# Kernel tuning notes

Hardware: AMD Instinct MI355X
Metric: run time of the kernel (lower is better)

The kernel has to match this reference:

```python
import jax, jax.numpy as jnp
import numpy as np


def setup_inputs() -> dict:
    key = jax.random.key(0)
    ks = jax.random.split(key, 5)
    t, b, s, d = 4, 4, 1024, 512
    x = jax.random.normal(ks[0], (t, b, s, d), dtype=jnp.float32)
    wq = jax.random.normal(ks[1], (d, d), dtype=jnp.float32) * 0.02
    wk = jax.random.normal(ks[2], (d, d), dtype=jnp.float32) * 0.02
    wv = jax.random.normal(ks[3], (d, d), dtype=jnp.float32) * 0.02
    wo = jax.random.normal(ks[4], (d, d), dtype=jnp.float32) * 0.02
    z = jnp.zeros((d,), dtype=jnp.float32)
    return {"x": x, "wq": wq, "bq": z, "wk": wk, "bk": z, "wv": wv,
            "bv": z, "wo": wo, "bo": z, "num_heads": 8}


def reference(x, wq, bq, wk, bk, wv, bv, wo, bo, num_heads):
    t, b, s, d = x.shape
    dh = d // num_heads
    # QKV projections (torch Linear stores weight as [out,in]; here weights are
    # random square matrices so x @ w + b is the same math)
    q = x @ wq + bq
    k = x @ wk + bk
    v = x @ wv + bv
    # Faithful to source: plain row-major view to (t*b*h, s, dh) WITHOUT
    # transposing a head axis (this mixes seq blocks into the batch-of-heads dim)
    q = q.reshape(t * b * num_heads, s, dh)
    k = k.reshape(t * b * num_heads, s, dh)
    v = v.reshape(t * b * num_heads, s, dh)
    scale = 1.0 / jnp.sqrt(jnp.float32(dh))
    scores = jnp.einsum('bqd,bkd->bqk', q, k) * scale  # [t*b*h, s, s]
    attn = jax.nn.softmax(scores, axis=-1)
    out = jnp.einsum('bqk,bkd->bqd', attn, v)  # [t*b*h, s, dh]
    out = out.reshape(t, b, s, d)
    return out @ wo + bo
```

## Files before the change

kernel.cpp:

```cpp
#include <hip/hip_runtime.h>

typedef __bf16 bf16;
typedef __bf16 bf16x4 __attribute__((ext_vector_type(4)));
typedef __bf16 bf16x8 __attribute__((ext_vector_type(8)));
typedef float  f32x4  __attribute__((ext_vector_type(4)));

#define MFMA16(a, b, c) __builtin_amdgcn_mfma_f32_16x16x32_bf16((a), (b), (c), 0, 0, 0)
#define SW(row, g) (((row) << 6) + ((((g) ^ ((row) & 7))) << 3))

#define QSCALE 0.1803368801111137f

typedef __attribute__((address_space(3))) uint32_t       lds_u32_t;
typedef const __attribute__((address_space(1))) uint32_t glob_u32_t;

__device__ __forceinline__ void ld_lds16(const bf16* g, bf16* l) {
    __builtin_amdgcn_global_load_lds((glob_u32_t*)g, (lds_u32_t*)l, 16, 0, 0);
}

__global__ __launch_bounds__(256) void prep(
    const float* __restrict__ X,
    const float* __restrict__ wq, const float* __restrict__ wk,
    const float* __restrict__ wv, const float* __restrict__ wo,
    bf16* __restrict__ Xb, bf16* __restrict__ wqkvT, bf16* __restrict__ woT)
{
    int bid = blockIdx.x;
    if (bid < 4096) {
        size_t i = ((size_t)bid * 256 + threadIdx.x) * 8;
        const f32x4* s = (const f32x4*)(X + i);
        f32x4 a = s[0], b = s[1];
        bf16x8 o;
        for (int e = 0; e < 4; e++) { o[e] = (bf16)a[e]; o[e + 4] = (bf16)b[e]; }
        *(bf16x8*)(Xb + i) = o;
    } else {
        int idx = (bid - 4096) * 256 + threadIdx.x;
        int which = idx >> 15;
        int r = idx & 32767;
        int kg = r >> 9, n = r & 511;
        const float* w = (which == 0) ? wq : (which == 1) ? wk : (which == 2) ? wv : wo;
        bf16x8 o;
        for (int e = 0; e < 8; e++) o[e] = (bf16)w[(size_t)(kg * 8 + e) * 512 + n];
        bf16* dst = ((which < 3) ? (wqkvT + (size_t)which * 262144) : woT) + (size_t)n * 512 + kg * 8;
        *(bf16x8*)dst = o;
    }
}

__global__ __launch_bounds__(256, 4) void gemm_qkv(
    const bf16* __restrict__ Xb, const bf16* __restrict__ WT,
    const float* __restrict__ bq, const float* __restrict__ bk,
    const float* __restrict__ bv,
    bf16* __restrict__ Q, bf16* __restrict__ K, bf16* __restrict__ V)
{
    __shared__ char smem[34816];
    bf16* As = (bf16*)smem;
    bf16* Bs = (bf16*)(smem + 16384);

    const int t = threadIdx.x;
    const int lane = t & 63, wid = t >> 6;
    const int wr = wid >> 1, wc = wid & 1;
    const int lr = lane & 15, quad = lane >> 4;
    const int bid = blockIdx.x;
    const int xcd = bid & 7, j0 = bid >> 3;
    const int m0 = (xcd * 16 + (j0 & 15)) * 128;
    const int x = j0 >> 4;
    const int which = x >> 2;
    const int n0 = (x & 3) * 128;
    const bf16* Wt = WT + (size_t)which * 262144;

    f32x4 zf = {0.f, 0.f, 0.f, 0.f};
    f32x4 acc[4][4];
    for (int i = 0; i < 4; i++)
        for (int jj = 0; jj < 4; jj++) acc[i][jj] = zf;

    const int srow = t >> 3;
    const int sg = (t & 7) ^ (srow & 7);
    const bf16* gA = Xb + (size_t)(m0 + srow) * 512 + sg * 8;
    const bf16* gB = Wt + (size_t)(n0 + srow) * 512 + sg * 8;
    bf16* lA = As + t * 8;
    bf16* lB = Bs + t * 8;

    for (int k0 = 0; k0 < 512; k0 += 64) {
        for (int p = 0; p < 4; p++) {
            ld_lds16(gA + k0 + p * 32 * 512, lA + p * 2048);
            ld_lds16(gB + k0 + p * 32 * 512, lB + p * 2048);
        }
        __syncthreads();
        for (int kk = 0; kk < 2; ++kk) {
            bf16x8 af[4], bf_[4];
            for (int i = 0; i < 4; i++)
                af[i] = *(const bf16x8*)&As[SW(wr * 64 + i * 16 + lr, kk * 4 + quad)];
            for (int jj = 0; jj < 4; jj++)
                bf_[jj] = *(const bf16x8*)&Bs[SW(wc * 64 + jj * 16 + lr, kk * 4 + quad)];
            for (int i = 0; i < 4; i++)
                for (int jj = 0; jj < 4; jj++)
                    acc[i][jj] = MFMA16(af[i], bf_[jj], acc[i][jj]);
        }
        __syncthreads();
    }

    bf16* OUT = (which == 0) ? Q : (which == 1) ? K : V;
    const float* bias = (which == 0) ? bq : (which == 1) ? bk : bv;
    const float qs = (which == 0) ? QSCALE : 1.0f;

    bf16* Ep = (bf16*)smem + wid * 4352;
    for (int jj = 0; jj < 4; jj++) {
        int n = n0 + wc * 64 + jj * 16 + lr;
        float bb = bias[n];
        for (int i = 0; i < 4; i++) {
            int row = i * 16 + quad * 4;
            for (int r = 0; r < 4; r++)
                Ep[(row + r) * 68 + jj * 16 + lr] = (bf16)((acc[i][jj][r] + bb) * qs);
        }
    }
    bf16* wO = OUT + (size_t)(m0 + wr * 64) * 512 + n0 + wc * 64;
    for (int s = 0; s < 8; s++) {
        int row = s * 8 + (lane >> 3), g = lane & 7;
        *(bf16x8*)(wO + (size_t)row * 512 + g * 8) = *(const bf16x8*)&Ep[row * 68 + g * 8];
    }
}

__global__ __launch_bounds__(256, 4) void gemm_out(
    const bf16* __restrict__ A, const bf16* __restrict__ WoT,
    const float* __restrict__ bo, float* __restrict__ OUT)
{
    __shared__ char smem[34816];
    bf16* As = (bf16*)smem;
    bf16* Bs = (bf16*)(smem + 16384);

    const int t = threadIdx.x;
    const int lane = t & 63, wid = t >> 6;
    const int wr = wid >> 1, wc = wid & 1;
    const int lr = lane & 15, quad = lane >> 4;
    const int bid = blockIdx.x;
    const int xcd = bid & 7, j0 = bid >> 3;
    const int m0 = (xcd * 16 + (j0 & 15)) * 128;
    const int n0 = (j0 >> 4) * 128;

    f32x4 zf = {0.f, 0.f, 0.f, 0.f};
    f32x4 acc[4][4];
    for (int i = 0; i < 4; i++)
        for (int jj = 0; jj < 4; jj++) acc[i][jj] = zf;

    const int srow = t >> 3;
    const int sg = (t & 7) ^ (srow & 7);
    const bf16* gA = A + (size_t)(m0 + srow) * 512 + sg * 8;
    const bf16* gB = WoT + (size_t)(n0 + srow) * 512 + sg * 8;
    bf16* lA = As + t * 8;
    bf16* lB = Bs + t * 8;

    for (int k0 = 0; k0 < 512; k0 += 64) {
        for (int p = 0; p < 4; p++) {
            ld_lds16(gA + k0 + p * 32 * 512, lA + p * 2048);
            ld_lds16(gB + k0 + p * 32 * 512, lB + p * 2048);
        }
        __syncthreads();
        for (int kk = 0; kk < 2; ++kk) {
            bf16x8 af[4], bf_[4];
            for (int i = 0; i < 4; i++)
                af[i] = *(const bf16x8*)&As[SW(wr * 64 + i * 16 + lr, kk * 4 + quad)];
            for (int jj = 0; jj < 4; jj++)
                bf_[jj] = *(const bf16x8*)&Bs[SW(wc * 64 + jj * 16 + lr, kk * 4 + quad)];
            for (int i = 0; i < 4; i++)
                for (int jj = 0; jj < 4; jj++)
                    acc[i][jj] = MFMA16(af[i], bf_[jj], acc[i][jj]);
        }
        __syncthreads();
    }

    float bb[4];
    for (int jj = 0; jj < 4; jj++) bb[jj] = bo[n0 + wc * 64 + jj * 16 + lr];

    float* Ef = (float*)smem + wid * 2112;
    for (int h = 0; h < 2; h++) {
        for (int jj = 0; jj < 4; jj++)
            for (int ii = 0; ii < 2; ii++) {
                int i = h * 2 + ii;
                int row = ii * 16 + quad * 4;
                for (int r = 0; r < 4; r++)
                    Ef[(row + r) * 66 + jj * 16 + lr] = acc[i][jj][r] + bb[jj];
            }
        float* wO = OUT + (size_t)(m0 + wr * 64 + h * 32) * 512 + n0 + wc * 64;
        for (int s = 0; s < 8; s++) {
            int row = s * 4 + (lane >> 4), c = (lane & 15) * 4;
            *(f32x4*)(wO + (size_t)row * 512 + c) = *(const f32x4*)&Ef[row * 66 + c];
        }
        __syncthreads();
    }
}

__global__ __launch_bounds__(256) void transpose_v(
    const bf16* __restrict__ V, bf16* __restrict__ VT)
{
    __shared__ bf16 L[64 * 72];
    const int t = threadIdx.x;
    const int b = blockIdx.y, kb = blockIdx.x;
    const bf16* src = V + ((size_t)b * 1024 + (size_t)kb * 64) * 64;
    const int row = t >> 2, c0 = (t & 3) * 16;
    *(bf16x8*)&L[row * 72 + c0]     = *(const bf16x8*)(src + row * 64 + c0);
    *(bf16x8*)&L[row * 72 + c0 + 8] = *(const bf16x8*)(src + row * 64 + c0 + 8);
    __syncthreads();
    bf16x8 o0, o1;
    for (int e = 0; e < 8; e++) {
        o0[e] = L[(c0 + e) * 72 + row];
        o1[e] = L[(c0 + 8 + e) * 72 + row];
    }
    bf16* dst = VT + ((size_t)b * 64 + row) * 1024 + (size_t)kb * 64 + c0;
    *(bf16x8*)dst       = o0;
    *(bf16x8*)(dst + 8) = o1;
}

__global__ __launch_bounds__(256, 4) void attn(
    const bf16* __restrict__ Q, const bf16* __restrict__ K,
    const bf16* __restrict__ VT, bf16* __restrict__ O)
{
    __shared__ char smem[32768];
    bf16* Kt = (bf16*)smem;
    bf16* Vt = (bf16*)(smem + 8192);
    bf16* Pt = (bf16*)(smem + 16384);

    const int t = threadIdx.x, lane = t & 63, wid = t >> 6;
    const int lr = lane & 15, quad = lane >> 4;
    const int bid = blockIdx.x;
    const int batch = (bid & 7) * 16 + ((bid >> 3) & 15);
    const int q0 = (bid >> 7) * 128;
    const bf16* Qb = Q + (size_t)batch * 65536;
    const bf16* Kb = K + (size_t)batch * 65536;
    const bf16* Vb = VT + (size_t)batch * 65536;

    bf16x8 qf[2][2];
    for (int jt = 0; jt < 2; jt++)
        for (int kk = 0; kk < 2; kk++)
            qf[jt][kk] = *(const bf16x8*)(Qb + (size_t)(q0 + wid * 32 + jt * 16 + lr) * 64 + kk * 32 + quad * 8);

    float lsum[2] = {0.f, 0.f};
    f32x4 zf = {0.f, 0.f, 0.f, 0.f};
    f32x4 oacc[2][4];
    for (int a = 0; a < 2; a++)
        for (int b = 0; b < 4; b++) oacc[a][b] = zf;

    const int vrow = t >> 2, vg = (t & 3) * 2;
    const bf16* gK = Kb + (size_t)vrow * 64 + (t & 3) * 16;
    const bf16* gV = Vb + (size_t)vrow * 1024 + (t & 3) * 16;

    bf16x8 kr0 = ((const bf16x8*)gK)[0], kr1 = ((const bf16x8*)gK)[1];
    bf16x8 vr0 = ((const bf16x8*)gV)[0], vr1 = ((const bf16x8*)gV)[1];

    for (int kt = 0; kt < 16; ++kt) {
        __syncthreads();
        *(bf16x8*)&Kt[SW(vrow, vg)]     = kr0;
        *(bf16x8*)&Kt[SW(vrow, vg + 1)] = kr1;
        *(bf16x8*)&Vt[SW(vrow, vg)]     = vr0;
        *(bf16x8*)&Vt[SW(vrow, vg + 1)] = vr1;
        __syncthreads();

        if (kt < 15) {
            const bf16x8* nK = (const bf16x8*)(gK + (kt + 1) * 4096);
            const bf16x8* nV = (const bf16x8*)(gV + (kt + 1) * 64);
            kr0 = nK[0]; kr1 = nK[1];
            vr0 = nV[0]; vr1 = nV[1];
        }

        f32x4 sacc[4][2];
        for (int i = 0; i < 4; i++)
            for (int jt = 0; jt < 2; jt++) sacc[i][jt] = zf;
        for (int kk = 0; kk < 2; ++kk) {
            bf16x8 af[4];
            for (int i = 0; i < 4; i++)
                af[i] = *(const bf16x8*)&Kt[SW(i * 16 + lr, kk * 4 + quad)];
            for (int i = 0; i < 4; i++)
                for (int jt = 0; jt < 2; jt++)
                    sacc[i][jt] = MFMA16(af[i], qf[jt][kk], sacc[i][jt]);
        }

        for (int jt = 0; jt < 2; jt++) {
            const int qrow = wid * 32 + jt * 16 + lr;
            const int pbase = (qrow << 6) + (quad & 1) * 4;
            float ss = 0.f;
            for (int i = 0; i < 4; i++) {
                bf16x4 pb;
                for (int r = 0; r < 4; r++) {
                    float p = __builtin_amdgcn_exp2f(sacc[i][jt][r]);
                    ss += p;
                    pb[r] = (bf16)p;
                }
                *(bf16x4*)&Pt[pbase + ((((i * 2 + (quad >> 1)) ^ (qrow & 7))) << 3)] = pb;
            }
            lsum[jt] += ss;
        }

        for (int kk = 0; kk < 2; ++kk) {
            bf16x8 ap[2], bv_[4];
            for (int mt = 0; mt < 2; mt++)
                ap[mt] = *(const bf16x8*)&Pt[SW(wid * 32 + mt * 16 + lr, kk * 4 + quad)];
            for (int nt = 0; nt < 4; nt++)
                bv_[nt] = *(const bf16x8*)&Vt[SW(nt * 16 + lr, kk * 4 + quad)];
            for (int mt = 0; mt < 2; mt++)
                for (int nt = 0; nt < 4; nt++)
                    oacc[mt][nt] = MFMA16(ap[mt], bv_[nt], oacc[mt][nt]);
        }
    }

    for (int jt = 0; jt < 2; jt++) {
        lsum[jt] += __shfl_xor(lsum[jt], 16, 64);
        lsum[jt] += __shfl_xor(lsum[jt], 32, 64);
    }
    float invl[2] = {1.f / lsum[0], 1.f / lsum[1]};

    __syncthreads();
    bf16* Ep = (bf16*)smem + wid * 2176;
    for (int mt = 0; mt < 2; mt++)
        for (int r = 0; r < 4; r++) {
            float im = __shfl(invl[mt], quad * 4 + r, 64);
            int row = mt * 16 + quad * 4 + r;
            for (int nt = 0; nt < 4; nt++)
                Ep[row * 68 + nt * 16 + lr] = (bf16)(oacc[mt][nt][r] * im);
        }
    bf16* Ob = O + (size_t)batch * 65536 + (size_t)(q0 + wid * 32) * 64;
    for (int s = 0; s < 4; s++) {
        int row = s * 8 + (lane >> 3), g = lane & 7;
        *(bf16x8*)(Ob + (size_t)row * 64 + g * 8) = *(const bf16x8*)&Ep[row * 68 + g * 8];
    }
}

extern "C" void kernel_launch(void* const* d_in, const int* in_sizes, int n_in,
                              void* d_out, int out_size, void* d_ws, size_t ws_size,
                              hipStream_t stream)
{
    const float* x  = (const float*)d_in[0];
    const float* wq = (const float*)d_in[1];
    const float* bq = (const float*)d_in[2];
    const float* wk = (const float*)d_in[3];
    const float* bk = (const float*)d_in[4];
    const float* wv = (const float*)d_in[5];
    const float* bv = (const float*)d_in[6];
    const float* wo = (const float*)d_in[7];
    const float* bo = (const float*)d_in[8];

    char* ws = (char*)d_ws;
    bf16* wqkvT = (bf16*)ws;
    bf16* woT   = (bf16*)(ws + 1572864);
    bf16* Xb    = (bf16*)(ws + 2097152);
    bf16* VTb   = Xb;
    bf16* Qb    = (bf16*)(ws + 2097152 + 16777216ull);
    bf16* Kb    = (bf16*)(ws + 2097152 + 2 * 16777216ull);
    bf16* Vb    = (bf16*)(ws + 2097152 + 3 * 16777216ull);
    bf16* Ab    = Vb;

    prep<<<4608, 256, 0, stream>>>(x, wq, wk, wv, wo, Xb, wqkvT, woT);
    gemm_qkv<<<1536, 256, 0, stream>>>(Xb, wqkvT, bq, bk, bv, Qb, Kb, Vb);
    transpose_v<<<dim3(16, 128), 256, 0, stream>>>(Vb, VTb);
    attn<<<1024, 256, 0, stream>>>(Qb, Kb, VTb, Ab);
    gemm_out<<<512, 256, 0, stream>>>(Ab, woT, bo, (float*)d_out);
}
```

Before: 208.9 us.

## Restructure attention loop with 32x32 MFMA, register-resident P, and async LDS double-buffering

Rewrites the attention inner loop. The 16x16 MFMAs become 32x32x16 MFMAs, and the probability tile stays in registers: it is converted with packed bf16 converts and rearranged with permlane32 swaps into the A-operand layout, so the P round-trip through LDS is gone. K and V tiles are now fetched with global_load_lds into double-buffered LDS, so the next tile's load overlaps compute and the register-staging copy disappears. Scheduling priority hints and explicit vmcnt waits are added; this relies on correct swizzle and lane-layout mapping and on LDS capacity.

```diff
diff --git a/kernel.cpp b/kernel.cpp
--- a/kernel.cpp
+++ b/kernel.cpp
@@ -4,8 +4,11 @@
 typedef __bf16 bf16x4 __attribute__((ext_vector_type(4)));
 typedef __bf16 bf16x8 __attribute__((ext_vector_type(8)));
 typedef float  f32x4  __attribute__((ext_vector_type(4)));
+typedef float  f32x16 __attribute__((ext_vector_type(16)));
+typedef unsigned int u32x4 __attribute__((ext_vector_type(4)));
 
 #define MFMA16(a, b, c) __builtin_amdgcn_mfma_f32_16x16x32_bf16((a), (b), (c), 0, 0, 0)
+#define MFMA32(a, b, c) __builtin_amdgcn_mfma_f32_32x32x16_bf16((a), (b), (c), 0, 0, 0)
 #define SW(row, g) (((row) << 6) + ((((g) ^ ((row) & 7))) << 3))
 
 #define QSCALE 0.1803368801111137f
@@ -213,12 +216,13 @@
     const bf16* __restrict__ VT, bf16* __restrict__ O)
 {
     __shared__ char smem[32768];
-    bf16* Kt = (bf16*)smem;
-    bf16* Vt = (bf16*)(smem + 8192);
-    bf16* Pt = (bf16*)(smem + 16384);
+    bf16* const K0 = (bf16*)smem;
+    bf16* const V0 = (bf16*)(smem + 8192);
+    bf16* const K1 = (bf16*)(smem + 16384);
+    bf16* const V1 = (bf16*)(smem + 24576);
 
     const int t = threadIdx.x, lane = t & 63, wid = t >> 6;
-    const int lr = lane & 15, quad = lane >> 4;
+    const int q31 = lane & 31, hi = lane >> 5;
     const int bid = blockIdx.x;
     const int batch = (bid & 7) * 16 + ((bid >> 3) & 15);
     const int q0 = (bid >> 7) * 128;
@@ -226,95 +230,119 @@
     const bf16* Kb = K + (size_t)batch * 65536;
     const bf16* Vb = VT + (size_t)batch * 65536;
 
-    bf16x8 qf[2][2];
-    for (int jt = 0; jt < 2; jt++)
-        for (int kk = 0; kk < 2; kk++)
-            qf[jt][kk] = *(const bf16x8*)(Qb + (size_t)(q0 + wid * 32 + jt * 16 + lr) * 64 + kk * 32 + quad * 8);
-
-    float lsum[2] = {0.f, 0.f};
-    f32x4 zf = {0.f, 0.f, 0.f, 0.f};
-    f32x4 oacc[2][4];
-    for (int a = 0; a < 2; a++)
-        for (int b = 0; b < 4; b++) oacc[a][b] = zf;
-
-    const int vrow = t >> 2, vg = (t & 3) * 2;
-    const bf16* gK = Kb + (size_t)vrow * 64 + (t & 3) * 16;
-    const bf16* gV = Vb + (size_t)vrow * 1024 + (t & 3) * 16;
-
-    bf16x8 kr0 = ((const bf16x8*)gK)[0], kr1 = ((const bf16x8*)gK)[1];
-    bf16x8 vr0 = ((const bf16x8*)gV)[0], vr1 = ((const bf16x8*)gV)[1];
+    bf16x8 qf[4];
+#pragma unroll
+    for (int kk = 0; kk < 4; ++kk)
+        qf[kk] = *(const bf16x8*)(Qb + (size_t)(q0 + wid * 32 + q31) * 64 + kk * 16 + hi * 8);
+
+    f32x16 oacc[2];
+#pragma unroll
+    for (int ct = 0; ct < 2; ++ct)
+#pragma unroll
+        for (int r = 0; r < 16; ++r) oacc[ct][r] = 0.f;
+    float lsum = 0.f;
+
+    const int srow = t >> 3;
+    const int sg8 = ((t & 7) ^ (srow & 7)) * 8;
+
+#define STAGE(ktile, KD, VD) do {                                        \
+        const bf16* gK_ = Kb + (size_t)(ktile) * 4096;                   \
+        const bf16* gV_ = Vb + (size_t)(ktile) * 64;                     \
+        ld_lds16(gK_ + srow * 64 + sg8,                  (KD) + t * 8);  \
+        ld_lds16(gK_ + (srow + 32) * 64 + sg8,           (KD) + t * 8 + 2048); \
+        ld_lds16(gV_ + (size_t)srow * 1024 + sg8,        (VD) + t * 8);  \
+        ld_lds16(gV_ + (size_t)(srow + 32) * 1024 + sg8, (VD) + t * 8 + 2048); \
+    } while (0)
+
+    STAGE(0, K0, V0);
 
     for (int kt = 0; kt < 16; ++kt) {
-        __syncthreads();
-        *(bf16x8*)&Kt[SW(vrow, vg)]     = kr0;
-        *(bf16x8*)&Kt[SW(vrow, vg + 1)] = kr1;
-        *(bf16x8*)&Vt[SW(vrow, vg)]     = vr0;
-        *(bf16x8*)&Vt[SW(vrow, vg + 1)] = vr1;
-        __syncthreads();
-
+        bf16* Kt = (kt & 1) ? K1 : K0;
+        bf16* Vt = (kt & 1) ? V1 : V0;
+        bf16* Kn = (kt & 1) ? K0 : K1;
+        bf16* Vn = (kt & 1) ? V0 : V1;
+
+        __builtin_amdgcn_sched_barrier(0);
+        __builtin_amdgcn_s_barrier();
+        __builtin_amdgcn_sched_barrier(0);
         if (kt < 15) {
-            const bf16x8* nK = (const bf16x8*)(gK + (kt + 1) * 4096);
-            const bf16x8* nV = (const bf16x8*)(gV + (kt + 1) * 64);
-            kr0 = nK[0]; kr1 = nK[1];
-            vr0 = nV[0]; vr1 = nV[1];
-        }
-
-        f32x4 sacc[4][2];
-        for (int i = 0; i < 4; i++)
-            for (int jt = 0; jt < 2; jt++) sacc[i][jt] = zf;
-        for (int kk = 0; kk < 2; ++kk) {
-            bf16x8 af[4];
-            for (int i = 0; i < 4; i++)
-                af[i] = *(const bf16x8*)&Kt[SW(i * 16 + lr, kk * 4 + quad)];
-            for (int i = 0; i < 4; i++)
-                for (int jt = 0; jt < 2; jt++)
-                    sacc[i][jt] = MFMA16(af[i], qf[jt][kk], sacc[i][jt]);
-        }
-
-        for (int jt = 0; jt < 2; jt++) {
-            const int qrow = wid * 32 + jt * 16 + lr;
-            const int pbase = (qrow << 6) + (quad & 1) * 4;
-            float ss = 0.f;
-            for (int i = 0; i < 4; i++) {
-                bf16x4 pb;
-                for (int r = 0; r < 4; r++) {
-                    float p = __builtin_amdgcn_exp2f(sacc[i][jt][r]);
-                    ss += p;
-                    pb[r] = (bf16)p;
-                }
-                *(bf16x4*)&Pt[pbase + ((((i * 2 + (quad >> 1)) ^ (qrow & 7))) << 3)] = pb;
+            STAGE(kt + 1, Kn, Vn);
+            asm volatile("s_waitcnt vmcnt(4)" ::: "memory");
+        } else {
+            asm volatile("s_waitcnt vmcnt(0)" ::: "memory");
+        }
+        __builtin_amdgcn_sched_barrier(0);
+        __builtin_amdgcn_s_barrier();
+        __builtin_amdgcn_sched_barrier(0);
+
+        f32x16 sacc[2];
+#pragma unroll
+        for (int i2 = 0; i2 < 2; ++i2)
+#pragma unroll
+            for (int r = 0; r < 16; ++r) sacc[i2][r] = 0.f;
+
+        __builtin_amdgcn_s_setprio(1);
+#pragma unroll
+        for (int kk = 0; kk < 4; ++kk) {
+            bf16x8 a0 = *(const bf16x8*)&Kt[SW(q31, kk * 2 + hi)];
+            bf16x8 a1 = *(const bf16x8*)&Kt[SW(32 + q31, kk * 2 + hi)];
+            sacc[0] = MFMA32(a0, qf[kk], sacc[0]);
+            sacc[1] = MFMA32(a1, qf[kk], sacc[1]);
+        }
+        __builtin_amdgcn_s_setprio(0);
+
+        float ls = 0.f;
+#pragma unroll
+        for (int i2 = 0; i2 < 2; ++i2)
+#pragma unroll
+            for (int r = 0; r < 16; ++r) {
+                float p = __builtin_amdgcn_exp2f(sacc[i2][r]);
+                ls += p;
+                sacc[i2][r] = p;
             }
-            lsum[jt] += ss;
-        }
-
-        for (int kk = 0; kk < 2; ++kk) {
-            bf16x8 ap[2], bv_[4];
-            for (int mt = 0; mt < 2; mt++)
-                ap[mt] = *(const bf16x8*)&Pt[SW(wid * 32 + mt * 16 + lr, kk * 4 + quad)];
-            for (int nt = 0; nt < 4; nt++)
-                bv_[nt] = *(const bf16x8*)&Vt[SW(nt * 16 + lr, kk * 4 + quad)];
-            for (int mt = 0; mt < 2; mt++)
-                for (int nt = 0; nt < 4; nt++)
-                    oacc[mt][nt] = MFMA16(ap[mt], bv_[nt], oacc[mt][nt]);
-        }
-    }
-
-    for (int jt = 0; jt < 2; jt++) {
-        lsum[jt] += __shfl_xor(lsum[jt], 16, 64);
-        lsum[jt] += __shfl_xor(lsum[jt], 32, 64);
-    }
-    float invl[2] = {1.f / lsum[0], 1.f / lsum[1]};
+        lsum += ls;
+
+        bf16x8 pa[4];
+#pragma unroll
+        for (int c = 0; c < 4; ++c) {
+            const int i2 = c >> 1, rb = (c & 1) * 8;
+            uint32_t x0, x1, x2, x3;
+            asm("v_cvt_pk_bf16_f32 %0, %1, %2" : "=v"(x0) : "v"(sacc[i2][rb + 0]), "v"(sacc[i2][rb + 1]));
+            asm("v_cvt_pk_bf16_f32 %0, %1, %2" : "=v"(x1) : "v"(sacc[i2][rb + 2]), "v"(sacc[i2][rb + 3]));
+            asm("v_cvt_pk_bf16_f32 %0, %1, %2" : "=v"(x2) : "v"(sacc[i2][rb + 4]), "v"(sacc[i2][rb + 5]));
+            asm("v_cvt_pk_bf16_f32 %0, %1, %2" : "=v"(x3) : "v"(sacc[i2][rb + 6]), "v"(sacc[i2][rb + 7]));
+            asm volatile("v_permlane32_swap_b32 %0, %1" : "+v"(x0), "+v"(x2));
+            asm volatile("v_permlane32_swap_b32 %0, %1" : "+v"(x1), "+v"(x3));
+            u32x4 w = {x0, x1, x2, x3};
+            pa[c] = __builtin_bit_cast(bf16x8, w);
+        }
+
+        __builtin_amdgcn_s_setprio(1);
+#pragma unroll
+        for (int c = 0; c < 4; ++c)
+#pragma unroll
+            for (int ct = 0; ct < 2; ++ct) {
+                bf16x8 bv = *(const bf16x8*)&Vt[SW(ct * 32 + q31, c * 2 + hi)];
+                oacc[ct] = MFMA32(pa[c], bv, oacc[ct]);
+            }
+        __builtin_amdgcn_s_setprio(0);
+    }
+#undef STAGE
+
+    lsum += __shfl_xor(lsum, 32, 64);
+    const float invl = 1.f / lsum;
 
     __syncthreads();
     bf16* Ep = (bf16*)smem + wid * 2176;
-    for (int mt = 0; mt < 2; mt++)
-        for (int r = 0; r < 4; r++) {
-            float im = __shfl(invl[mt], quad * 4 + r, 64);
-            int row = mt * 16 + quad * 4 + r;
-            for (int nt = 0; nt < 4; nt++)
-                Ep[row * 68 + nt * 16 + lr] = (bf16)(oacc[mt][nt][r] * im);
-        }
+#pragma unroll
+    for (int r = 0; r < 16; ++r) {
+        const int ql = (r & 3) + 8 * (r >> 2) + 4 * hi;
+        const float im = __shfl(invl, ql, 64);
+        Ep[ql * 68 + q31]      = (bf16)(oacc[0][r] * im);
+        Ep[ql * 68 + 32 + q31] = (bf16)(oacc[1][r] * im);
+    }
     bf16* Ob = O + (size_t)batch * 65536 + (size_t)(q0 + wid * 32) * 64;
+#pragma unroll
     for (int s = 0; s < 4; s++) {
         int row = s * 8 + (lane >> 3), g = lane & 7;
         *(bf16x8*)(Ob + (size_t)row * 64 + g * 8) = *(const bf16x8*)&Ep[row * 68 + g * 8];
```

Result: faster. 202.5 us (-3.0%).
